# Performance work log

Hardware: AMD Instinct MI355X
Metric: run time of the kernel (lower is better)

Reference implementation:

```python
import jax, jax.numpy as jnp
import numpy as np

N_NODES = 20000
N_EDGES = 640000
F = 64       # n_features
B = 20       # n_basis
LN_EPS = 1e-5

act = jax.nn.silu

def _lin_init(key, fan_in, fan_out):
    return jax.random.normal(key, (fan_in, fan_out), dtype=jnp.float32) / np.sqrt(fan_in)

def setup_inputs() -> dict:
    key = jax.random.key(0)
    ks = jax.random.split(key, 18)
    inp = {
        "atom_node": jax.random.normal(ks[0], (N_NODES, F), dtype=jnp.float32),
        "force_node": jax.random.normal(ks[1], (N_NODES, 3, F), dtype=jnp.float32),
        "dir_edge": jax.random.normal(ks[2], (N_EDGES, 3), dtype=jnp.float32),
        "dist_edge": jax.random.uniform(ks[3], (N_EDGES, B), dtype=jnp.float32),
        "edge_index": jax.random.randint(ks[4], (2, N_EDGES), 0, N_NODES, dtype=jnp.int64),
        # message_nodepart: Linear(F,F)+act+Linear(F,F)
        "W1": _lin_init(ks[5], F, F), "b1": jnp.zeros((F,), jnp.float32),
        "W2": _lin_init(ks[6], F, F), "b2": jnp.zeros((F,), jnp.float32),
        # message_edgepart: Linear(B,F,bias=False)
        "We": _lin_init(ks[7], B, F),
        # equiv_message1/2: Linear(F,F,nobias)+act+Linear(F,F,nobias)
        "Wq1a": _lin_init(ks[8], F, F), "Wq1b": _lin_init(ks[9], F, F),
        "Wq2a": _lin_init(ks[10], F, F), "Wq2b": _lin_init(ks[11], F, F),
        # equiv_update: Linear(F,F,nobias)
        "Wu": _lin_init(ks[12], F, F),
        # LayerNorm(F)
        "gamma": jnp.ones((F,), jnp.float32), "beta": jnp.zeros((F,), jnp.float32),
    }
    return inp

def reference(atom_node, force_node, dir_edge, dist_edge, edge_index,
              W1, b1, W2, b2, We, Wq1a, Wq1b, Wq2a, Wq2b, Wu, gamma, beta):
    src, dst = edge_index[0], edge_index[1]
    n = atom_node.shape[0]

    # node part of the message: MLP over nodes [N,F]
    mn = act(atom_node @ W1 + b1) @ W2 + b2
    # edge part: [E,F]
    me = dist_edge @ We
    # message: elementwise product of edge part and both endpoint node parts [E,F]
    message = me * mn[src] * mn[dst]

    # invariant update: scatter-add messages to source nodes
    inv_update1 = jax.ops.segment_sum(message, src, num_segments=n)
    atom_node = atom_node + inv_update1

    # equivariant messages [E,3,F]
    em1_inv = act(message @ Wq1a) @ Wq1b            # [E,F]
    em2_inv = act(message @ Wq2a) @ Wq2b            # [E,F]
    equiv_msg = (em1_inv[:, None, :] * dir_edge[:, :, None]
                 + em2_inv[:, None, :] * force_node[dst])  # [E,3,F]
    force_update = jax.ops.segment_sum(equiv_msg, src, num_segments=n)
    force_node = force_node + force_update

    # invariant contraction of vector features: sum over the 3-dim
    inv_update2 = jnp.sum(force_node * (force_node @ Wu), axis=1)  # [N,F]
    atom_node = atom_node + inv_update2

    # LayerNorm over feature dim
    mu = jnp.mean(atom_node, axis=-1, keepdims=True)
    var = jnp.var(atom_node, axis=-1, keepdims=True)
    atom_node = (atom_node - mu) * jax.lax.rsqrt(var + LN_EPS) * gamma + beta

    return (atom_node, force_node)
```

## Files before the change

### kernel.cpp

```cpp
#include <hip/hip_runtime.h>

#define N_NODES 20000
#define N_EDGES 640000
#define FDIM 64
#define NB 20
#define LN_EPS 1e-5f

typedef __attribute__((ext_vector_type(8))) short bf16x8;
typedef __attribute__((ext_vector_type(4))) float f32x4;

#define SEL_HI 0x07060302u
#define SEL_LO 0x05040100u
#define MFMA16 __builtin_amdgcn_mfma_f32_16x16x32_bf16

__device__ __forceinline__ float silu_f(float x) { return x / (1.0f + __expf(-x)); }

__device__ __forceinline__ float bcast_lane(float v, int lane) {
    return __int_as_float(__builtin_amdgcn_readlane(__float_as_int(v), lane));
}

__device__ __forceinline__ unsigned bf16_rn(float x) {
    unsigned u = __float_as_uint(x);
    return (u + 0x7FFFu + ((u >> 16) & 1u)) >> 16;
}

__device__ __forceinline__ unsigned pack_split(float x) {
    unsigned h = bf16_rn(x);
    unsigned lo = bf16_rn(x - __uint_as_float(h << 16));
    return (h << 16) | lo;
}

__device__ __forceinline__ void load_afrag(const unsigned* rowPtr, int kh, int q,
                                           bf16x8* ahi, bf16x8* alo) {
    const uint4 ra = *(const uint4*)(rowPtr + kh * 32 + q * 8);
    const uint4 rb = *(const uint4*)(rowPtr + kh * 32 + q * 8 + 4);
    union { unsigned u[4]; bf16x8 v; } H, L;
    H.u[0] = __builtin_amdgcn_perm(ra.y, ra.x, SEL_HI);
    H.u[1] = __builtin_amdgcn_perm(ra.w, ra.z, SEL_HI);
    H.u[2] = __builtin_amdgcn_perm(rb.y, rb.x, SEL_HI);
    H.u[3] = __builtin_amdgcn_perm(rb.w, rb.z, SEL_HI);
    L.u[0] = __builtin_amdgcn_perm(ra.y, ra.x, SEL_LO);
    L.u[1] = __builtin_amdgcn_perm(ra.w, ra.z, SEL_LO);
    L.u[2] = __builtin_amdgcn_perm(rb.y, rb.x, SEL_LO);
    L.u[3] = __builtin_amdgcn_perm(rb.w, rb.z, SEL_LO);
    *ahi = H.v;
    *alo = L.v;
}

__device__ __forceinline__ void mm3(const unsigned* Bhi, const unsigned* Blo,
                                    bf16x8 ahi, bf16x8 alo, f32x4* acc, int kh, int l) {
#pragma unroll
    for (int c = 0; c < 4; ++c) {
        bf16x8 bh = *(const bf16x8*)(Bhi + (kh * 4 + c) * 256 + l * 4);
        bf16x8 bl = *(const bf16x8*)(Blo + (kh * 4 + c) * 256 + l * 4);
        acc[c] = MFMA16(ahi, bh, acc[c], 0, 0, 0);
        acc[c] = MFMA16(ahi, bl, acc[c], 0, 0, 0);
        acc[c] = MFMA16(alo, bh, acc[c], 0, 0, 0);
    }
}

__global__ __launch_bounds__(256) void node_mlp_kernel(
    const float* __restrict__ atom, const float* __restrict__ W1, const float* __restrict__ b1,
    const float* __restrict__ W2, const float* __restrict__ b2, float* __restrict__ mn)
{
    __shared__ float W1s[FDIM][FDIM];
    __shared__ float W2s[FDIM][FDIM];
    const int f = threadIdx.x, ty = threadIdx.y;
    const int tid = ty * 64 + f;
    for (int i = tid; i < FDIM * FDIM; i += 256) {
        ((float*)W1s)[i] = W1[i];
        ((float*)W2s)[i] = W2[i];
    }
    __syncthreads();
    const float bb1 = b1[f], bb2 = b2[f];
    const int nw = gridDim.x * 4;
    for (int n = blockIdx.x * 4 + ty; n < N_NODES; n += nw) {
        const float a = atom[n * FDIM + f];
        float h = bb1;
        for (int g = 0; g < FDIM; ++g) h += bcast_lane(a, g) * W1s[g][f];
        h = silu_f(h);
        float o = bb2;
        for (int g = 0; g < FDIM; ++g) o += bcast_lane(h, g) * W2s[g][f];
        mn[n * FDIM + f] = o;
    }
}

__global__ __launch_bounds__(1024) void edge_kernel(
    const float* __restrict__ dist,
    const float* __restrict__ dir,
    const int* __restrict__ eidx,
    const float* __restrict__ mn,
    const float* __restrict__ We,
    const float* __restrict__ Wq1a, const float* __restrict__ Wq1b,
    const float* __restrict__ Wq2a, const float* __restrict__ Wq2b,
    const float* __restrict__ forceN,
    float* __restrict__ atomAcc,
    float* __restrict__ forceAcc)
{
    __shared__ __align__(16) unsigned Bfr[16384];
    __shared__ __align__(16) unsigned Astg[16][16][76];

    const int l = threadIdx.x;
    const int ty = threadIdx.y;
    const int q = l >> 4, row = l & 15;

    for (int t = ty; t < 32; t += 16) {
        const int mm = t >> 3, kh = (t >> 2) & 1, c = t & 3;
        const float* W = (mm == 0) ? Wq1a : (mm == 1) ? Wq2a : (mm == 2) ? Wq1b : Wq2b;
        const int n = c * 16 + row;
        const int kb = kh * 32 + q * 8;
        unsigned* hiP = &Bfr[(((mm * 2 + 0) * 2 + kh) * 4 + c) * 256 + l * 4];
        unsigned* loP = &Bfr[(((mm * 2 + 1) * 2 + kh) * 4 + c) * 256 + l * 4];
#pragma unroll
        for (int i = 0; i < 4; ++i) {
            float w0 = W[(kb + 2 * i) * FDIM + n];
            float w1 = W[(kb + 2 * i + 1) * FDIM + n];
            unsigned h0 = bf16_rn(w0);
            unsigned l0 = bf16_rn(w0 - __uint_as_float(h0 << 16));
            unsigned h1 = bf16_rn(w1);
            unsigned l1 = bf16_rn(w1 - __uint_as_float(h1 << 16));
            hiP[i] = h0 | (h1 << 16);
            loP[i] = l0 | (l1 << 16);
        }
    }
    __syncthreads();

    const unsigned* B1aH = Bfr + 0 * 2048; const unsigned* B1aL = Bfr + 1 * 2048;
    const unsigned* B2aH = Bfr + 2 * 2048; const unsigned* B2aL = Bfr + 3 * 2048;
    const unsigned* B1bH = Bfr + 4 * 2048; const unsigned* B1bL = Bfr + 5 * 2048;
    const unsigned* B2bH = Bfr + 6 * 2048; const unsigned* B2bL = Bfr + 7 * 2048;

    float we[NB];
#pragma unroll
    for (int b = 0; b < NB; ++b) we[b] = We[b * FDIM + l];

    unsigned* stg = &Astg[ty][0][0];
    const unsigned* rowPtr = &Astg[ty][row][0];

    const int ngroups = N_EDGES / 16;
    const int stride = gridDim.x * 16;
    for (int grp = blockIdx.x * 16 + ty; grp < ngroups; grp += stride) {
        const int e0 = grp * 16;

#pragma unroll
        for (int j = 0; j < 16; ++j) {
            const int src = __builtin_amdgcn_readfirstlane(eidx[e0 + j]);
            const int dst = __builtin_amdgcn_readfirstlane(eidx[N_EDGES + e0 + j]);
            float me = 0.0f;
#pragma unroll
            for (int b = 0; b < NB; ++b) me += dist[(e0 + j) * NB + b] * we[b];
            const float m = me * mn[src * FDIM + l] * mn[dst * FDIM + l];
            atomicAdd(&atomAcc[src * FDIM + l], m);
            stg[j * 76 + l] = pack_split(m);
        }

        f32x4 acc1[4], acc2[4];
#pragma unroll
        for (int c = 0; c < 4; ++c) {
            acc1[c] = (f32x4){0.f, 0.f, 0.f, 0.f};
            acc2[c] = (f32x4){0.f, 0.f, 0.f, 0.f};
        }
#pragma unroll
        for (int kh = 0; kh < 2; ++kh) {
            bf16x8 ahi, alo;
            load_afrag(rowPtr, kh, q, &ahi, &alo);
            mm3(B1aH, B1aL, ahi, alo, acc1, kh, l);
            mm3(B2aH, B2aL, ahi, alo, acc2, kh, l);
        }
#pragma unroll
        for (int c = 0; c < 4; ++c)
#pragma unroll
            for (int r = 0; r < 4; ++r) {
                acc1[c][r] = silu_f(acc1[c][r]);
                acc2[c][r] = silu_f(acc2[c][r]);
            }

#pragma unroll
        for (int c = 0; c < 4; ++c)
#pragma unroll
            for (int r = 0; r < 4; ++r)
                stg[(q * 4 + r) * 76 + (row + 16 * c)] = pack_split(acc1[c][r]);

        f32x4 eacc1[4];
#pragma unroll
        for (int c = 0; c < 4; ++c) eacc1[c] = (f32x4){0.f, 0.f, 0.f, 0.f};
#pragma unroll
        for (int kh = 0; kh < 2; ++kh) {
            bf16x8 ahi, alo;
            load_afrag(rowPtr, kh, q, &ahi, &alo);
            mm3(B1bH, B1bL, ahi, alo, eacc1, kh, l);
        }

#pragma unroll
        for (int c = 0; c < 4; ++c)
#pragma unroll
            for (int r = 0; r < 4; ++r)
                stg[(q * 4 + r) * 76 + (row + 16 * c)] = pack_split(acc2[c][r]);

        f32x4 eacc2[4];
#pragma unroll
        for (int c = 0; c < 4; ++c) eacc2[c] = (f32x4){0.f, 0.f, 0.f, 0.f};
#pragma unroll
        for (int kh = 0; kh < 2; ++kh) {
            bf16x8 ahi, alo;
            load_afrag(rowPtr, kh, q, &ahi, &alo);
            mm3(B2bH, B2bL, ahi, alo, eacc2, kh, l);
        }

#pragma unroll
        for (int r = 0; r < 4; ++r) {
            const int em = e0 + q * 4 + r;
            const int vs = eidx[em];
            const int vd = eidx[N_EDGES + em];
            const float d0 = dir[em * 3 + 0];
            const float d1 = dir[em * 3 + 1];
            const float d2 = dir[em * 3 + 2];
            const float* fd = forceN + (size_t)vd * 3 * FDIM;
            float* fa = forceAcc + (size_t)vs * 3 * FDIM;
#pragma unroll
            for (int c = 0; c < 4; ++c) {
                const int n = row + 16 * c;
                const float a = eacc1[c][r];
                const float b = eacc2[c][r];
                atomicAdd(&fa[0 * FDIM + n], a * d0 + b * fd[0 * FDIM + n]);
                atomicAdd(&fa[1 * FDIM + n], a * d1 + b * fd[1 * FDIM + n]);
                atomicAdd(&fa[2 * FDIM + n], a * d2 + b * fd[2 * FDIM + n]);
            }
        }
    }
}

__global__ __launch_bounds__(256) void node_final_kernel(
    const float* __restrict__ Wu, const float* __restrict__ gamma, const float* __restrict__ beta,
    float* __restrict__ atomAcc,
    const float* __restrict__ forceOut)
{
    __shared__ float Wus[FDIM][FDIM];
    const int f = threadIdx.x, ty = threadIdx.y;
    const int tid = ty * 64 + f;
    for (int i = tid; i < FDIM * FDIM; i += 256) ((float*)Wus)[i] = Wu[i];
    __syncthreads();
    const float gg = gamma[f], bb = beta[f];
    const int nw = gridDim.x * 4;
    for (int n = blockIdx.x * 4 + ty; n < N_NODES; n += nw) {
        const float f0 = forceOut[((size_t)n * 3 + 0) * FDIM + f];
        const float f1 = forceOut[((size_t)n * 3 + 1) * FDIM + f];
        const float f2 = forceOut[((size_t)n * 3 + 2) * FDIM + f];
        float r0 = 0.0f, r1 = 0.0f, r2 = 0.0f;
#pragma unroll 8
        for (int g = 0; g < FDIM; ++g) {
            const float w = Wus[g][f];
            r0 += bcast_lane(f0, g) * w;
            r1 += bcast_lane(f1, g) * w;
            r2 += bcast_lane(f2, g) * w;
        }
        float a = atomAcc[n * FDIM + f] + (f0 * r0 + f1 * r1 + f2 * r2);
        float s = a;
#pragma unroll
        for (int off = 32; off >= 1; off >>= 1) s += __shfl_xor(s, off, 64);
        const float mu = s * (1.0f / 64.0f);
        const float d = a - mu;
        float v = d * d;
#pragma unroll
        for (int off = 32; off >= 1; off >>= 1) v += __shfl_xor(v, off, 64);
        v *= (1.0f / 64.0f);
        atomAcc[n * FDIM + f] = d * rsqrtf(v + LN_EPS) * gg + bb;
    }
}

extern "C" void kernel_launch(void* const* d_in, const int* in_sizes, int n_in,
                              void* d_out, int out_size, void* d_ws, size_t ws_size,
                              hipStream_t stream)
{
    const float* atom_node  = (const float*)d_in[0];
    const float* force_node = (const float*)d_in[1];
    const float* dir_edge   = (const float*)d_in[2];
    const float* dist_edge  = (const float*)d_in[3];
    const int*   edge_index = (const int*)d_in[4];
    const float* W1   = (const float*)d_in[5];
    const float* b1   = (const float*)d_in[6];
    const float* W2   = (const float*)d_in[7];
    const float* b2   = (const float*)d_in[8];
    const float* We   = (const float*)d_in[9];
    const float* Wq1a = (const float*)d_in[10];
    const float* Wq1b = (const float*)d_in[11];
    const float* Wq2a = (const float*)d_in[12];
    const float* Wq2b = (const float*)d_in[13];
    const float* Wu   = (const float*)d_in[14];
    const float* gamma = (const float*)d_in[15];
    const float* beta  = (const float*)d_in[16];

    float* atomOut  = (float*)d_out;
    float* forceOut = (float*)d_out + (size_t)N_NODES * FDIM;
    float* mn = (float*)d_ws;

    hipMemcpyAsync(atomOut, atom_node, (size_t)N_NODES * FDIM * sizeof(float),
                   hipMemcpyDeviceToDevice, stream);
    hipMemcpyAsync(forceOut, force_node, (size_t)N_NODES * 3 * FDIM * sizeof(float),
                   hipMemcpyDeviceToDevice, stream);

    dim3 blk4(64, 4);
    dim3 blk16(64, 16);
    node_mlp_kernel<<<512, blk4, 0, stream>>>(atom_node, W1, b1, W2, b2, mn);
    edge_kernel<<<256, blk16, 0, stream>>>(dist_edge, dir_edge, edge_index, mn, We,
                                           Wq1a, Wq1b, Wq2a, Wq2b, force_node,
                                           atomOut, forceOut);
    node_final_kernel<<<512, blk4, 0, stream>>>(Wu, gamma, beta, atomOut, forceOut);
}
```

Before: 634.7 us.

## Compute edge distance projection with split-bf16 MFMA and load edge metadata once per group

Replaces the per-lane scalar 20-term dot product of dist_edge with We by a split-bf16 MFMA. We is pre-split into LDS fragments and dist is loaded as float4 tiles per 16-edge group. Edge indices and directions are now loaded cooperatively once per group and shared through readlane and shuffles, instead of being reloaded with redundant scalar and global loads. In exchange it adds LDS usage and staging traffic, and the split-bf16 product may differ slightly in precision from the fp32 FMA chain.

```diff
diff --git a/kernel.cpp b/kernel.cpp
--- a/kernel.cpp
+++ b/kernel.cpp
@@ -98,6 +98,7 @@
     float* __restrict__ forceAcc)
 {
     __shared__ __align__(16) unsigned Bfr[16384];
+    __shared__ __align__(16) unsigned WeFr[2048];
     __shared__ __align__(16) unsigned Astg[16][16][76];
 
     const int l = threadIdx.x;
@@ -123,16 +124,30 @@
             loP[i] = l0 | (l1 << 16);
         }
     }
+    for (int c = ty; c < 4; c += 16) {
+        const int n = c * 16 + row;
+        unsigned* hiP = &WeFr[(0 * 4 + c) * 256 + l * 4];
+        unsigned* loP = &WeFr[(1 * 4 + c) * 256 + l * 4];
+#pragma unroll
+        for (int i = 0; i < 4; ++i) {
+            const int k0 = q * 8 + 2 * i, k1 = k0 + 1;
+            float w0 = (k0 < NB) ? We[k0 * FDIM + n] : 0.0f;
+            float w1 = (k1 < NB) ? We[k1 * FDIM + n] : 0.0f;
+            unsigned h0 = bf16_rn(w0);
+            unsigned l0 = bf16_rn(w0 - __uint_as_float(h0 << 16));
+            unsigned h1 = bf16_rn(w1);
+            unsigned l1 = bf16_rn(w1 - __uint_as_float(h1 << 16));
+            hiP[i] = h0 | (h1 << 16);
+            loP[i] = l0 | (l1 << 16);
+        }
+    }
     __syncthreads();
 
     const unsigned* B1aH = Bfr + 0 * 2048; const unsigned* B1aL = Bfr + 1 * 2048;
     const unsigned* B2aH = Bfr + 2 * 2048; const unsigned* B2aL = Bfr + 3 * 2048;
     const unsigned* B1bH = Bfr + 4 * 2048; const unsigned* B1bL = Bfr + 5 * 2048;
     const unsigned* B2bH = Bfr + 6 * 2048; const unsigned* B2bL = Bfr + 7 * 2048;
-
-    float we[NB];
-#pragma unroll
-    for (int b = 0; b < NB; ++b) we[b] = We[b * FDIM + l];
+    const unsigned* WeH = WeFr;            const unsigned* WeL = WeFr + 1024;
 
     unsigned* stg = &Astg[ty][0][0];
     const unsigned* rowPtr = &Astg[ty][row][0];
@@ -142,13 +157,44 @@
     for (int grp = blockIdx.x * 16 + ty; grp < ngroups; grp += stride) {
         const int e0 = grp * 16;
 
+        int ev = 0;
+        if (l < 32) ev = eidx[(l < 16) ? (e0 + l) : (N_EDGES + e0 + (l - 16))];
+        float dv = (l < 48) ? dir[e0 * 3 + l] : 0.0f;
+
+        const float* dp = dist + (size_t)(e0 + row) * NB + q * 8;
+        float4 da = {0.f, 0.f, 0.f, 0.f}, db = {0.f, 0.f, 0.f, 0.f};
+        if (q < 2)       { da = *(const float4*)dp; db = *(const float4*)(dp + 4); }
+        else if (q == 2) { da = *(const float4*)dp; }
+        unsigned s0 = pack_split(da.x), s1 = pack_split(da.y);
+        unsigned s2 = pack_split(da.z), s3 = pack_split(da.w);
+        unsigned s4 = pack_split(db.x), s5 = pack_split(db.y);
+        unsigned s6 = pack_split(db.z), s7 = pack_split(db.w);
+        union { unsigned u[4]; bf16x8 v; } AH, AL;
+        AH.u[0] = __builtin_amdgcn_perm(s1, s0, SEL_HI);
+        AH.u[1] = __builtin_amdgcn_perm(s3, s2, SEL_HI);
+        AH.u[2] = __builtin_amdgcn_perm(s5, s4, SEL_HI);
+        AH.u[3] = __builtin_amdgcn_perm(s7, s6, SEL_HI);
+        AL.u[0] = __builtin_amdgcn_perm(s1, s0, SEL_LO);
+        AL.u[1] = __builtin_amdgcn_perm(s3, s2, SEL_LO);
+        AL.u[2] = __builtin_amdgcn_perm(s5, s4, SEL_LO);
+        AL.u[3] = __builtin_amdgcn_perm(s7, s6, SEL_LO);
+
+        f32x4 me4[4];
+#pragma unroll
+        for (int c = 0; c < 4; ++c) me4[c] = (f32x4){0.f, 0.f, 0.f, 0.f};
+        mm3(WeH, WeL, AH.v, AL.v, me4, 0, l);
+
+#pragma unroll
+        for (int c = 0; c < 4; ++c)
+#pragma unroll
+            for (int r = 0; r < 4; ++r)
+                stg[(q * 4 + r) * 76 + (row + 16 * c)] = __float_as_uint(me4[c][r]);
+
 #pragma unroll
         for (int j = 0; j < 16; ++j) {
-            const int src = __builtin_amdgcn_readfirstlane(eidx[e0 + j]);
-            const int dst = __builtin_amdgcn_readfirstlane(eidx[N_EDGES + e0 + j]);
-            float me = 0.0f;
-#pragma unroll
-            for (int b = 0; b < NB; ++b) me += dist[(e0 + j) * NB + b] * we[b];
+            const int src = __builtin_amdgcn_readlane(ev, j);
+            const int dst = __builtin_amdgcn_readlane(ev, 16 + j);
+            const float me = __uint_as_float(stg[j * 76 + l]);
             const float m = me * mn[src * FDIM + l] * mn[dst * FDIM + l];
             atomicAdd(&atomAcc[src * FDIM + l], m);
             stg[j * 76 + l] = pack_split(m);
@@ -209,12 +255,12 @@
 
 #pragma unroll
         for (int r = 0; r < 4; ++r) {
-            const int em = e0 + q * 4 + r;
-            const int vs = eidx[em];
-            const int vd = eidx[N_EDGES + em];
-            const float d0 = dir[em * 3 + 0];
-            const float d1 = dir[em * 3 + 1];
-            const float d2 = dir[em * 3 + 2];
+            const int eo = q * 4 + r;
+            const int vs = __shfl(ev, eo);
+            const int vd = __shfl(ev, 16 + eo);
+            const float d0 = __shfl(dv, eo * 3 + 0);
+            const float d1 = __shfl(dv, eo * 3 + 1);
+            const float d2 = __shfl(dv, eo * 3 + 2);
             const float* fd = forceN + (size_t)vd * 3 * FDIM;
             float* fa = forceAcc + (size_t)vs * 3 * FDIM;
 #pragma unroll
```

Result: faster. 606.8 us (-4.4%).
